# Kernel optimization log

Hardware: AMD Instinct MI355X
Metric: run time of the kernel (lower is better)

Reference implementation:

```python
import jax, jax.numpy as jnp
import numpy as np

N = 100000
E = 640000
D = 128


def _sage_conv(x, src, dst, Wp, bp, Wl, bl, Wr):
    # project=True: project + relu source features before aggregation
    h = jax.nn.relu(x @ Wp.T + bp)            # [N, D]
    msgs = h[src]                              # [E, D] gather
    summed = jax.ops.segment_sum(msgs, dst, num_segments=N)   # [N, D]
    cnt = jax.ops.segment_sum(jnp.ones((msgs.shape[0],), x.dtype), dst, num_segments=N)
    mean = summed / jnp.maximum(cnt, 1.0)[:, None]
    # lin_l on aggregated neighbors (with bias) + lin_r on root (no bias)
    return mean @ Wl.T + bl + x @ Wr.T


def setup_inputs() -> dict:
    key = jax.random.key(0)
    ks = jax.random.split(key, 16)
    s = 1.0 / np.sqrt(D)
    x = jax.random.normal(ks[0], (N, D), dtype=jnp.float32)
    edge_index = jax.random.randint(ks[1], (2, E), 0, N, dtype=jnp.int64)
    params = {}
    for i, base in enumerate(["conv0", "conv1"]):
        params[base + "_Wp"] = jax.random.uniform(ks[2 + 5 * i], (D, D), jnp.float32, -s, s)
        params[base + "_bp"] = jax.random.uniform(ks[3 + 5 * i], (D,), jnp.float32, -s, s)
        params[base + "_Wl"] = jax.random.uniform(ks[4 + 5 * i], (D, D), jnp.float32, -s, s)
        params[base + "_bl"] = jax.random.uniform(ks[5 + 5 * i], (D,), jnp.float32, -s, s)
        params[base + "_Wr"] = jax.random.uniform(ks[6 + 5 * i], (D, D), jnp.float32, -s, s)
    return {"x": x, "edge_index": edge_index, **params}


def reference(x, edge_index,
              conv0_Wp, conv0_bp, conv0_Wl, conv0_bl, conv0_Wr,
              conv1_Wp, conv1_bp, conv1_Wl, conv1_bl, conv1_Wr):
    src, dst = edge_index[0], edge_index[1]
    h = _sage_conv(x, src, dst, conv0_Wp, conv0_bp, conv0_Wl, conv0_bl, conv0_Wr)
    h = jax.nn.relu(h)
    return _sage_conv(h, src, dst, conv1_Wp, conv1_bp, conv1_Wl, conv1_bl, conv1_Wr)
```

## Files before the change

### kernel.cpp

```cpp
#include <hip/hip_runtime.h>

#define DD 128

typedef _Float16 f16;
typedef __attribute__((ext_vector_type(8))) _Float16 v8h;
typedef __attribute__((ext_vector_type(4))) _Float16 v4h;
typedef __attribute__((ext_vector_type(2))) _Float16 f16x2;
typedef __attribute__((ext_vector_type(4))) float f32x4;

static inline int cdiv(int a, int b) { return (a + b - 1) / b; }


__global__ __launch_bounds__(256) void zero_kernel(int* __restrict__ p, int n) {
    int i = blockIdx.x * 256 + threadIdx.x;
    if (i < n) p[i] = 0;
}


__global__ __launch_bounds__(256) void count_kernel(const int* __restrict__ dst, int E,
                                                    int* __restrict__ cnt) {
    int e = blockIdx.x * 256 + threadIdx.x;
    if (e < E) atomicAdd(&cnt[dst[e]], 1);
}

__global__ __launch_bounds__(256) void scan1(const int* __restrict__ cnt, int N,
                                             int* __restrict__ bsum) {
    __shared__ int s[256];
    int i = blockIdx.x * 256 + threadIdx.x;
    s[threadIdx.x] = (i < N) ? cnt[i] : 0;
    __syncthreads();
    for (int off = 128; off > 0; off >>= 1) {
        if (threadIdx.x < off) s[threadIdx.x] += s[threadIdx.x + off];
        __syncthreads();
    }
    if (threadIdx.x == 0) bsum[blockIdx.x] = s[0];
}

__global__ __launch_bounds__(512) void scan2(const int* __restrict__ bsum, int NB,
                                             int* __restrict__ boff) {
    __shared__ int s[512];
    int t = threadIdx.x;
    int v = (t < NB) ? bsum[t] : 0;
    s[t] = v;
    __syncthreads();
    for (int off = 1; off < 512; off <<= 1) {
        int x = (t >= off) ? s[t - off] : 0;
        __syncthreads();
        s[t] += x;
        __syncthreads();
    }
    if (t < NB) boff[t] = s[t] - v;
}

__global__ __launch_bounds__(256) void scan3(const int* __restrict__ cnt,
                                             const int* __restrict__ boff, int N,
                                             int* __restrict__ off) {
    __shared__ int s[256];
    int t = threadIdx.x;
    int i = blockIdx.x * 256 + t;
    int v = (i < N) ? cnt[i] : 0;
    s[t] = v;
    __syncthreads();
    for (int o = 1; o < 256; o <<= 1) {
        int x = (t >= o) ? s[t - o] : 0;
        __syncthreads();
        s[t] += x;
        __syncthreads();
    }
    int excl = s[t] - v + boff[blockIdx.x];
    if (i < N) off[i] = excl;
    if (i == N - 1) off[N] = excl + v;
}

__global__ __launch_bounds__(256) void fill_kernel(const int* __restrict__ src,
                                                   const int* __restrict__ dst, int E,
                                                   const int* __restrict__ off,
                                                   int* __restrict__ cnt,
                                                   int* __restrict__ csr) {
    int e = blockIdx.x * 256 + threadIdx.x;
    if (e < E) {
        int d = dst[e];
        int p = atomicSub(&cnt[d], 1) - 1;
        csr[off[d] + p] = src[e];
    }
}


__global__ __launch_bounds__(256) void cvt_w_kernel(const float* __restrict__ W0,
                                                    const float* __restrict__ W1,
                                                    const float* __restrict__ W2,
                                                    const float* __restrict__ W3,
                                                    const float* __restrict__ W4,
                                                    const float* __restrict__ W5,
                                                    f16* __restrict__ out) {
    int mat = blockIdx.x >> 4;
    const float* W = mat == 0 ? W0 : mat == 1 ? W1 : mat == 2 ? W2
                   : mat == 3 ? W3 : mat == 4 ? W4 : W5;
    int base = (blockIdx.x & 15) * 1024 + threadIdx.x * 4;
    float4 v = *(const float4*)(W + base);
    v4h o;
    o[0] = (f16)v.x; o[1] = (f16)v.y; o[2] = (f16)v.z; o[3] = (f16)v.w;
    *(v4h*)(out + mat * 16384 + base) = o;
}

__global__ __launch_bounds__(256) void cvt_x_kernel(const float* __restrict__ x,
                                                    f16* __restrict__ out, int n8) {
    int i = blockIdx.x * 256 + threadIdx.x;
    if (i >= n8) return;
    float4 a = *(const float4*)(x + (size_t)i * 8);
    float4 b = *(const float4*)(x + (size_t)i * 8 + 4);
    v8h r;
    r[0] = (f16)a.x; r[1] = (f16)a.y; r[2] = (f16)a.z; r[3] = (f16)a.w;
    r[4] = (f16)b.x; r[5] = (f16)b.y; r[6] = (f16)b.z; r[7] = (f16)b.w;
    *(v8h*)(out + (size_t)i * 8) = r;
}


__global__ __launch_bounds__(256) void aggregate_kernel(const f16* __restrict__ h,
                                                        const int* __restrict__ off,
                                                        const int* __restrict__ csr,
                                                        f16* __restrict__ mean, int N) {
    int n = blockIdx.x * 4 + (threadIdx.x >> 6);
    int l = threadIdx.x & 63;
    int g = l >> 4, c = l & 15;
    if (n >= N) return;
    int s = off[n], e = off[n + 1];
    float acc[8] = {0.f, 0.f, 0.f, 0.f, 0.f, 0.f, 0.f, 0.f};
    for (int i = s + g; i < e; i += 4) {
        int idx = csr[i];
        v8h v = *(const v8h*)(h + (size_t)idx * DD + c * 8);
#pragma unroll
        for (int j = 0; j < 8; ++j) acc[j] += (float)v[j];
    }
#pragma unroll
    for (int j = 0; j < 8; ++j) {
        acc[j] += __shfl_xor(acc[j], 16);
        acc[j] += __shfl_xor(acc[j], 32);
    }
    int deg = e - s;
    float inv = 1.0f / (float)(deg > 0 ? deg : 1);
    if (g == 0) {
        v8h o;
#pragma unroll
        for (int j = 0; j < 8; ++j) o[j] = (f16)(acc[j] * inv);
        *(v8h*)(mean + (size_t)n * DD + c * 8) = o;
    }
}


__device__ inline void stage_w(const f16* __restrict__ Wg, f16* __restrict__ smem, int t) {
#pragma unroll
    for (int i = 0; i < 8; ++i) {
        int idx16 = i * 256 + t;
        int col = idx16 >> 4, c16 = idx16 & 15;
        int sc = c16 ^ (col & 7);
        uint4 v = *(const uint4*)(Wg + idx16 * 8);
        *(uint4*)(smem + col * DD + sc * 8) = v;
    }
}

__device__ inline v8h read_b(const f16* __restrict__ smem, int ct, int ki, int l) {
    int col = ct * 16 + (l & 15);
    int c16 = ki * 4 + (l >> 4);
    int sc = c16 ^ (col & 7);
    return *(const v8h*)(smem + col * DD + sc * 8);
}

__device__ inline v8h load_frag16(const f16* __restrict__ A, int row, int kb, int M) {
    if (row >= M) {
        v8h z = {};
        return z;
    }
    return *(const v8h*)(A + (size_t)row * DD + kb);
}


__global__ __launch_bounds__(256) void proj_gemm(const f16* __restrict__ A,
                                                 const f16* __restrict__ W1,
                                                 const float* __restrict__ bias,
                                                 f16* __restrict__ OUT, int M) {
    __shared__ f16 WS[DD * DD];
    int t = threadIdx.x, l = t & 63, w = t >> 6;
    int row0 = blockIdx.x * 128 + w * 32;
    int r = l & 15, cg = l >> 4;

    stage_w(W1, WS, t);

    v8h af[2][4];
#pragma unroll
    for (int rt = 0; rt < 2; ++rt)
#pragma unroll
        for (int ki = 0; ki < 4; ++ki)
            af[rt][ki] = load_frag16(A, row0 + rt * 16 + r, ki * 32 + cg * 8, M);
    __syncthreads();

    f32x4 acc[2][8];
#pragma unroll
    for (int ct = 0; ct < 8; ++ct) {
        float bv = bias[ct * 16 + r];
        f32x4 b4 = {bv, bv, bv, bv};
        acc[0][ct] = b4;
        acc[1][ct] = b4;
    }

#pragma unroll
    for (int ct = 0; ct < 8; ++ct)
#pragma unroll
        for (int ki = 0; ki < 4; ++ki) {
            v8h b = read_b(WS, ct, ki, l);
            acc[0][ct] = __builtin_amdgcn_mfma_f32_16x16x32_f16(af[0][ki], b, acc[0][ct], 0, 0, 0);
            acc[1][ct] = __builtin_amdgcn_mfma_f32_16x16x32_f16(af[1][ki], b, acc[1][ct], 0, 0, 0);
        }

#pragma unroll
    for (int rt = 0; rt < 2; ++rt)
#pragma unroll
        for (int ct = 0; ct < 8; ++ct)
#pragma unroll
            for (int j = 0; j < 4; ++j) {
                int row = row0 + rt * 16 + cg * 4 + j;
                if (row < M)
                    OUT[(size_t)row * DD + ct * 16 + r] = (f16)fmaxf(acc[rt][ct][j], 0.f);
            }
}


template <typename TO, bool RELU>
__global__ __launch_bounds__(256) void dual_gemm(const f16* __restrict__ A,
                                                 const f16* __restrict__ Wl,
                                                 const float* __restrict__ bias,
                                                 const f16* __restrict__ B,
                                                 const f16* __restrict__ Wr,
                                                 TO* __restrict__ OUT, int M) {
    __shared__ f16 WS[DD * DD];
    int t = threadIdx.x, l = t & 63, w = t >> 6;
    int row0 = blockIdx.x * 128 + w * 32;
    int r = l & 15, cg = l >> 4;

    stage_w(Wl, WS, t);

    v8h afA[2][4], afB[2][4];
#pragma unroll
    for (int rt = 0; rt < 2; ++rt)
#pragma unroll
        for (int ki = 0; ki < 4; ++ki) {
            int row = row0 + rt * 16 + r, kb = ki * 32 + cg * 8;
            afA[rt][ki] = load_frag16(A, row, kb, M);
            afB[rt][ki] = load_frag16(B, row, kb, M);
        }
    __syncthreads();

    f32x4 acc[2][8];
#pragma unroll
    for (int ct = 0; ct < 8; ++ct) {
        float bv = bias[ct * 16 + r];
        f32x4 b4 = {bv, bv, bv, bv};
        acc[0][ct] = b4;
        acc[1][ct] = b4;
    }

#pragma unroll
    for (int ct = 0; ct < 8; ++ct)
#pragma unroll
        for (int ki = 0; ki < 4; ++ki) {
            v8h b = read_b(WS, ct, ki, l);
            acc[0][ct] = __builtin_amdgcn_mfma_f32_16x16x32_f16(afA[0][ki], b, acc[0][ct], 0, 0, 0);
            acc[1][ct] = __builtin_amdgcn_mfma_f32_16x16x32_f16(afA[1][ki], b, acc[1][ct], 0, 0, 0);
        }

    __syncthreads();
    stage_w(Wr, WS, t);
    __syncthreads();

#pragma unroll
    for (int ct = 0; ct < 8; ++ct)
#pragma unroll
        for (int ki = 0; ki < 4; ++ki) {
            v8h b = read_b(WS, ct, ki, l);
            acc[0][ct] = __builtin_amdgcn_mfma_f32_16x16x32_f16(afB[0][ki], b, acc[0][ct], 0, 0, 0);
            acc[1][ct] = __builtin_amdgcn_mfma_f32_16x16x32_f16(afB[1][ki], b, acc[1][ct], 0, 0, 0);
        }

#pragma unroll
    for (int rt = 0; rt < 2; ++rt)
#pragma unroll
        for (int ct = 0; ct < 8; ++ct)
#pragma unroll
            for (int j = 0; j < 4; ++j) {
                int row = row0 + rt * 16 + cg * 4 + j;
                if (row < M) {
                    float v = acc[rt][ct][j];
                    if (RELU) v = fmaxf(v, 0.f);
                    OUT[(size_t)row * DD + ct * 16 + r] = (TO)v;
                }
            }
}


__global__ __launch_bounds__(256) void dualproj_gemm(const f16* __restrict__ A,
                                                     const f16* __restrict__ Wl,
                                                     const float* __restrict__ bl,
                                                     const f16* __restrict__ B,
                                                     const f16* __restrict__ Wr,
                                                     f16* __restrict__ Y,
                                                     const f16* __restrict__ Wp,
                                                     const float* __restrict__ bp,
                                                     f16* __restrict__ H, int M) {
    __shared__ f16 WS[DD * DD];
    int t = threadIdx.x, l = t & 63, w = t >> 6;
    int row0 = blockIdx.x * 128 + w * 32;
    int r = l & 15, cg = l >> 4;

    stage_w(Wl, WS, t);

    v8h afA[2][4], afB[2][4];
#pragma unroll
    for (int rt = 0; rt < 2; ++rt)
#pragma unroll
        for (int ki = 0; ki < 4; ++ki) {
            int row = row0 + rt * 16 + r, kb = ki * 32 + cg * 8;
            afA[rt][ki] = load_frag16(A, row, kb, M);
            afB[rt][ki] = load_frag16(B, row, kb, M);
        }
    __syncthreads();

    f32x4 acc[2][8];
#pragma unroll
    for (int ct = 0; ct < 8; ++ct) {
        float bv = bl[ct * 16 + r];
        f32x4 b4 = {bv, bv, bv, bv};
        acc[0][ct] = b4;
        acc[1][ct] = b4;
    }

#pragma unroll
    for (int ct = 0; ct < 8; ++ct)
#pragma unroll
        for (int ki = 0; ki < 4; ++ki) {
            v8h b = read_b(WS, ct, ki, l);
            acc[0][ct] = __builtin_amdgcn_mfma_f32_16x16x32_f16(afA[0][ki], b, acc[0][ct], 0, 0, 0);
            acc[1][ct] = __builtin_amdgcn_mfma_f32_16x16x32_f16(afA[1][ki], b, acc[1][ct], 0, 0, 0);
        }

    __syncthreads();
    stage_w(Wr, WS, t);
    __syncthreads();

#pragma unroll
    for (int ct = 0; ct < 8; ++ct)
#pragma unroll
        for (int ki = 0; ki < 4; ++ki) {
            v8h b = read_b(WS, ct, ki, l);
            acc[0][ct] = __builtin_amdgcn_mfma_f32_16x16x32_f16(afB[0][ki], b, acc[0][ct], 0, 0, 0);
            acc[1][ct] = __builtin_amdgcn_mfma_f32_16x16x32_f16(afB[1][ki], b, acc[1][ct], 0, 0, 0);
        }

    __syncthreads();
#pragma unroll
    for (int rt = 0; rt < 2; ++rt)
#pragma unroll
        for (int ct = 0; ct < 8; ++ct)
#pragma unroll
            for (int j = 0; j < 4; ++j) {
                int brow = w * 32 + rt * 16 + cg * 4 + j;
                int col = ct * 16 + r;
                f16 hv = (f16)fmaxf(acc[rt][ct][j], 0.f);
                int c16 = col >> 3;
                WS[brow * DD + (((c16 ^ (brow & 7)) << 3) | (col & 7))] = hv;
                int grow = blockIdx.x * 128 + brow;
                if (grow < M) Y[(size_t)grow * DD + col] = hv;
            }
    __syncthreads();

    v8h af2[2][4];
#pragma unroll
    for (int rt = 0; rt < 2; ++rt)
#pragma unroll
        for (int ki = 0; ki < 4; ++ki) {
            int brow = w * 32 + rt * 16 + r;
            af2[rt][ki] = *(const v8h*)(WS + brow * DD + (((ki * 4 + cg) ^ (brow & 7)) << 3));
        }
    __syncthreads();

    stage_w(Wp, WS, t);

    f32x4 acc2[2][8];
#pragma unroll
    for (int ct = 0; ct < 8; ++ct) {
        float bv = bp[ct * 16 + r];
        f32x4 b4 = {bv, bv, bv, bv};
        acc2[0][ct] = b4;
        acc2[1][ct] = b4;
    }
    __syncthreads();

#pragma unroll
    for (int ct = 0; ct < 8; ++ct)
#pragma unroll
        for (int ki = 0; ki < 4; ++ki) {
            v8h b = read_b(WS, ct, ki, l);
            acc2[0][ct] = __builtin_amdgcn_mfma_f32_16x16x32_f16(af2[0][ki], b, acc2[0][ct], 0, 0, 0);
            acc2[1][ct] = __builtin_amdgcn_mfma_f32_16x16x32_f16(af2[1][ki], b, acc2[1][ct], 0, 0, 0);
        }

#pragma unroll
    for (int rt = 0; rt < 2; ++rt)
#pragma unroll
        for (int ct = 0; ct < 8; ++ct)
#pragma unroll
            for (int j = 0; j < 4; ++j) {
                int row = row0 + rt * 16 + cg * 4 + j;
                if (row < M)
                    H[(size_t)row * DD + ct * 16 + r] = (f16)fmaxf(acc2[rt][ct][j], 0.f);
            }
}


extern "C" void kernel_launch(void* const* d_in, const int* in_sizes, int n_in,
                              void* d_out, int out_size, void* d_ws, size_t ws_size,
                              hipStream_t stream) {
    const float* x = (const float*)d_in[0];
    const int* ei = (const int*)d_in[1];
    const float* Wp0 = (const float*)d_in[2];
    const float* bp0 = (const float*)d_in[3];
    const float* Wl0 = (const float*)d_in[4];
    const float* bl0 = (const float*)d_in[5];
    const float* Wr0 = (const float*)d_in[6];
    const float* Wp1 = (const float*)d_in[7];
    const float* bp1 = (const float*)d_in[8];
    const float* Wl1 = (const float*)d_in[9];
    const float* bl1 = (const float*)d_in[10];
    const float* Wr1 = (const float*)d_in[11];

    int N = in_sizes[0] / DD;
    int E = in_sizes[1] / 2;
    const int* src = ei;
    const int* dst = ei + E;

    char* ws = (char*)d_ws;
    size_t o = 0;
    auto alloc = [&](size_t bytes) {
        size_t r = o;
        o = (o + bytes + 255) & ~(size_t)255;
        return r;
    };
    f16* w16 = (f16*)(ws + alloc((size_t)6 * DD * DD * 2));
    int* cnt = (int*)(ws + alloc((size_t)N * 4));
    int* off = (int*)(ws + alloc((size_t)(N + 1) * 4));
    int NB = cdiv(N, 256);
    int* bsum = (int*)(ws + alloc((size_t)NB * 4));
    int* boff = (int*)(ws + alloc((size_t)NB * 4));
    int* csr = (int*)(ws + alloc((size_t)E * 4));
    f16* mean = (f16*)(ws + alloc((size_t)N * DD * 2));
    f16* y1 = (f16*)(ws + alloc((size_t)N * DD * 2));
    f16* h = (f16*)d_out;
    f16* x16 = (f16*)((char*)d_out + (size_t)N * DD * 2);
    (void)ws_size;

    zero_kernel<<<NB, 256, 0, stream>>>(cnt, N);
    count_kernel<<<cdiv(E, 256), 256, 0, stream>>>(dst, E, cnt);
    scan1<<<NB, 256, 0, stream>>>(cnt, N, bsum);
    scan2<<<1, 512, 0, stream>>>(bsum, NB, boff);
    scan3<<<NB, 256, 0, stream>>>(cnt, boff, N, off);
    fill_kernel<<<cdiv(E, 256), 256, 0, stream>>>(src, dst, E, off, cnt, csr);

    cvt_w_kernel<<<96, 256, 0, stream>>>(Wp0, Wl0, Wr0, Wp1, Wl1, Wr1, w16);
    const f16* wp0 = w16 + 0 * 16384;
    const f16* wl0 = w16 + 1 * 16384;
    const f16* wr0 = w16 + 2 * 16384;
    const f16* wp1 = w16 + 3 * 16384;
    const f16* wl1 = w16 + 4 * 16384;
    const f16* wr1 = w16 + 5 * 16384;

    cvt_x_kernel<<<cdiv(N * DD / 8, 256), 256, 0, stream>>>(x, x16, N * DD / 8);

    int GB = cdiv(N, 128);
    proj_gemm<<<GB, 256, 0, stream>>>(x16, wp0, bp0, h, N);
    aggregate_kernel<<<cdiv(N, 4), 256, 0, stream>>>(h, off, csr, mean, N);
    dualproj_gemm<<<GB, 256, 0, stream>>>(mean, wl0, bl0, x16, wr0, y1, wp1, bp1, h, N);
    aggregate_kernel<<<cdiv(N, 4), 256, 0, stream>>>(h, off, csr, mean, N);
    dual_gemm<float, false><<<GB, 256, 0, stream>>>(mean, wl1, bl1, y1, wr1, (float*)d_out, N);
}
```

Before: 243.0 us.

## Fuse CSR build and conversions into fewer launches with atomic-cursor offsets

After: 257.6 us. 6.0% more time.

```diff
diff --git a/kernel.cpp b/kernel.cpp
--- a/kernel.cpp
+++ b/kernel.cpp
@@ -5,7 +5,6 @@
 typedef _Float16 f16;
 typedef __attribute__((ext_vector_type(8))) _Float16 v8h;
 typedef __attribute__((ext_vector_type(4))) _Float16 v4h;
-typedef __attribute__((ext_vector_type(2))) _Float16 f16x2;
 typedef __attribute__((ext_vector_type(4))) float f32x4;
 
 static inline int cdiv(int a, int b) { return (a + b - 1) / b; }
@@ -17,45 +16,47 @@
 }
 
 
-__global__ __launch_bounds__(256) void count_kernel(const int* __restrict__ dst, int E,
-                                                    int* __restrict__ cnt) {
-    int e = blockIdx.x * 256 + threadIdx.x;
-    if (e < E) atomicAdd(&cnt[dst[e]], 1);
-}
-
-__global__ __launch_bounds__(256) void scan1(const int* __restrict__ cnt, int N,
-                                             int* __restrict__ bsum) {
+__global__ __launch_bounds__(256) void bigprep_kernel(
+    const float* __restrict__ x, f16* __restrict__ x16, int n8,
+    const float* __restrict__ W0, const float* __restrict__ W1,
+    const float* __restrict__ W2, const float* __restrict__ W3,
+    const float* __restrict__ W4, const float* __restrict__ W5,
+    f16* __restrict__ w16,
+    const int* __restrict__ dst, int E, int* __restrict__ cnt,
+    int nbx) {
+    int b = blockIdx.x;
+    if (b < nbx) {
+        int i = b * 256 + threadIdx.x;
+        if (i >= n8) return;
+        float4 a = *(const float4*)(x + (size_t)i * 8);
+        float4 c = *(const float4*)(x + (size_t)i * 8 + 4);
+        v8h r;
+        r[0] = (f16)a.x; r[1] = (f16)a.y; r[2] = (f16)a.z; r[3] = (f16)a.w;
+        r[4] = (f16)c.x; r[5] = (f16)c.y; r[6] = (f16)c.z; r[7] = (f16)c.w;
+        *(v8h*)(x16 + (size_t)i * 8) = r;
+    } else if (b < nbx + 96) {
+        int bb = b - nbx;
+        int mat = bb >> 4;
+        const float* W = mat == 0 ? W0 : mat == 1 ? W1 : mat == 2 ? W2
+                       : mat == 3 ? W3 : mat == 4 ? W4 : W5;
+        int base = (bb & 15) * 1024 + threadIdx.x * 4;
+        float4 v = *(const float4*)(W + base);
+        v4h o;
+        o[0] = (f16)v.x; o[1] = (f16)v.y; o[2] = (f16)v.z; o[3] = (f16)v.w;
+        *(v4h*)(w16 + mat * 16384 + base) = o;
+    } else {
+        int e = (b - nbx - 96) * 256 + threadIdx.x;
+        if (e < E) atomicAdd(&cnt[dst[e]], 1);
+    }
+}
+
+
+__global__ __launch_bounds__(256) void offs_kernel(const int* __restrict__ cnt, int N,
+                                                   int* __restrict__ off,
+                                                   int* __restrict__ deg,
+                                                   int* __restrict__ cursor) {
     __shared__ int s[256];
-    int i = blockIdx.x * 256 + threadIdx.x;
-    s[threadIdx.x] = (i < N) ? cnt[i] : 0;
-    __syncthreads();
-    for (int off = 128; off > 0; off >>= 1) {
-        if (threadIdx.x < off) s[threadIdx.x] += s[threadIdx.x + off];
-        __syncthreads();
-    }
-    if (threadIdx.x == 0) bsum[blockIdx.x] = s[0];
-}
-
-__global__ __launch_bounds__(512) void scan2(const int* __restrict__ bsum, int NB,
-                                             int* __restrict__ boff) {
-    __shared__ int s[512];
-    int t = threadIdx.x;
-    int v = (t < NB) ? bsum[t] : 0;
-    s[t] = v;
-    __syncthreads();
-    for (int off = 1; off < 512; off <<= 1) {
-        int x = (t >= off) ? s[t - off] : 0;
-        __syncthreads();
-        s[t] += x;
-        __syncthreads();
-    }
-    if (t < NB) boff[t] = s[t] - v;
-}
-
-__global__ __launch_bounds__(256) void scan3(const int* __restrict__ cnt,
-                                             const int* __restrict__ boff, int N,
-                                             int* __restrict__ off) {
-    __shared__ int s[256];
+    __shared__ int base;
     int t = threadIdx.x;
     int i = blockIdx.x * 256 + t;
     int v = (i < N) ? cnt[i] : 0;
@@ -67,64 +68,112 @@
         s[t] += x;
         __syncthreads();
     }
-    int excl = s[t] - v + boff[blockIdx.x];
-    if (i < N) off[i] = excl;
-    if (i == N - 1) off[N] = excl + v;
-}
-
-__global__ __launch_bounds__(256) void fill_kernel(const int* __restrict__ src,
-                                                   const int* __restrict__ dst, int E,
-                                                   const int* __restrict__ off,
-                                                   int* __restrict__ cnt,
-                                                   int* __restrict__ csr) {
-    int e = blockIdx.x * 256 + threadIdx.x;
-    if (e < E) {
-        int d = dst[e];
-        int p = atomicSub(&cnt[d], 1) - 1;
-        csr[off[d] + p] = src[e];
-    }
-}
-
-
-__global__ __launch_bounds__(256) void cvt_w_kernel(const float* __restrict__ W0,
-                                                    const float* __restrict__ W1,
-                                                    const float* __restrict__ W2,
-                                                    const float* __restrict__ W3,
-                                                    const float* __restrict__ W4,
-                                                    const float* __restrict__ W5,
-                                                    f16* __restrict__ out) {
-    int mat = blockIdx.x >> 4;
-    const float* W = mat == 0 ? W0 : mat == 1 ? W1 : mat == 2 ? W2
-                   : mat == 3 ? W3 : mat == 4 ? W4 : W5;
-    int base = (blockIdx.x & 15) * 1024 + threadIdx.x * 4;
-    float4 v = *(const float4*)(W + base);
-    v4h o;
-    o[0] = (f16)v.x; o[1] = (f16)v.y; o[2] = (f16)v.z; o[3] = (f16)v.w;
-    *(v4h*)(out + mat * 16384 + base) = o;
-}
-
-__global__ __launch_bounds__(256) void cvt_x_kernel(const float* __restrict__ x,
-                                                    f16* __restrict__ out, int n8) {
-    int i = blockIdx.x * 256 + threadIdx.x;
-    if (i >= n8) return;
-    float4 a = *(const float4*)(x + (size_t)i * 8);
-    float4 b = *(const float4*)(x + (size_t)i * 8 + 4);
-    v8h r;
-    r[0] = (f16)a.x; r[1] = (f16)a.y; r[2] = (f16)a.z; r[3] = (f16)a.w;
-    r[4] = (f16)b.x; r[5] = (f16)b.y; r[6] = (f16)b.z; r[7] = (f16)b.w;
-    *(v8h*)(out + (size_t)i * 8) = r;
+    if (t == 255) base = atomicAdd(cursor, s[255]);
+    __syncthreads();
+    if (i < N) {
+        off[i] = base + s[t] - v;
+        deg[i] = v;
+    }
+}
+
+
+__device__ inline void stage_w(const f16* __restrict__ Wg, f16* __restrict__ smem, int t) {
+#pragma unroll
+    for (int i = 0; i < 8; ++i) {
+        int idx16 = i * 256 + t;
+        int col = idx16 >> 4, c16 = idx16 & 15;
+        int sc = c16 ^ (col & 7);
+        uint4 v = *(const uint4*)(Wg + idx16 * 8);
+        *(uint4*)(smem + col * DD + sc * 8) = v;
+    }
+}
+
+__device__ inline v8h read_b(const f16* __restrict__ smem, int ct, int ki, int l) {
+    int col = ct * 16 + (l & 15);
+    int c16 = ki * 4 + (l >> 4);
+    int sc = c16 ^ (col & 7);
+    return *(const v8h*)(smem + col * DD + sc * 8);
+}
+
+__device__ inline v8h load_frag16(const f16* __restrict__ A, int row, int kb, int M) {
+    if (row >= M) {
+        v8h z = {};
+        return z;
+    }
+    return *(const v8h*)(A + (size_t)row * DD + kb);
+}
+
+
+__global__ __launch_bounds__(256) void fuse1_kernel(
+    const f16* __restrict__ A, const f16* __restrict__ W1,
+    const float* __restrict__ bias, f16* __restrict__ OUT, int M, int GB,
+    const int* __restrict__ src, const int* __restrict__ dst, int E,
+    const int* __restrict__ off, int* __restrict__ cnt, int* __restrict__ csr) {
+    __shared__ f16 WS[DD * DD];
+    if (blockIdx.x >= (unsigned)GB) {
+        int e = (blockIdx.x - GB) * 256 + threadIdx.x;
+        if (e < E) {
+            int d = dst[e];
+            int p = atomicSub(&cnt[d], 1) - 1;
+            csr[off[d] + p] = src[e];
+        }
+        return;
+    }
+    int t = threadIdx.x, l = t & 63, w = t >> 6;
+    int row0 = blockIdx.x * 128 + w * 32;
+    int r = l & 15, cg = l >> 4;
+
+    stage_w(W1, WS, t);
+
+    v8h af[2][4];
+#pragma unroll
+    for (int rt = 0; rt < 2; ++rt)
+#pragma unroll
+        for (int ki = 0; ki < 4; ++ki)
+            af[rt][ki] = load_frag16(A, row0 + rt * 16 + r, ki * 32 + cg * 8, M);
+    __syncthreads();
+
+    f32x4 acc[2][8];
+#pragma unroll
+    for (int ct = 0; ct < 8; ++ct) {
+        float bv = bias[ct * 16 + r];
+        f32x4 b4 = {bv, bv, bv, bv};
+        acc[0][ct] = b4;
+        acc[1][ct] = b4;
+    }
+
+#pragma unroll
+    for (int ct = 0; ct < 8; ++ct)
+#pragma unroll
+        for (int ki = 0; ki < 4; ++ki) {
+            v8h b = read_b(WS, ct, ki, l);
+            acc[0][ct] = __builtin_amdgcn_mfma_f32_16x16x32_f16(af[0][ki], b, acc[0][ct], 0, 0, 0);
+            acc[1][ct] = __builtin_amdgcn_mfma_f32_16x16x32_f16(af[1][ki], b, acc[1][ct], 0, 0, 0);
+        }
+
+#pragma unroll
+    for (int rt = 0; rt < 2; ++rt)
+#pragma unroll
+        for (int ct = 0; ct < 8; ++ct)
+#pragma unroll
+            for (int j = 0; j < 4; ++j) {
+                int row = row0 + rt * 16 + cg * 4 + j;
+                if (row < M)
+                    OUT[(size_t)row * DD + ct * 16 + r] = (f16)fmaxf(acc[rt][ct][j], 0.f);
+            }
 }
 
 
 __global__ __launch_bounds__(256) void aggregate_kernel(const f16* __restrict__ h,
                                                         const int* __restrict__ off,
+                                                        const int* __restrict__ deg,
                                                         const int* __restrict__ csr,
                                                         f16* __restrict__ mean, int N) {
     int n = blockIdx.x * 4 + (threadIdx.x >> 6);
     int l = threadIdx.x & 63;
     int g = l >> 4, c = l & 15;
     if (n >= N) return;
-    int s = off[n], e = off[n + 1];
+    int s = off[n], d = deg[n], e = s + d;
     float acc[8] = {0.f, 0.f, 0.f, 0.f, 0.f, 0.f, 0.f, 0.f};
     for (int i = s + g; i < e; i += 4) {
         int idx = csr[i];
@@ -137,91 +186,13 @@
         acc[j] += __shfl_xor(acc[j], 16);
         acc[j] += __shfl_xor(acc[j], 32);
     }
-    int deg = e - s;
-    float inv = 1.0f / (float)(deg > 0 ? deg : 1);
+    float inv = 1.0f / (float)(d > 0 ? d : 1);
     if (g == 0) {
         v8h o;
 #pragma unroll
         for (int j = 0; j < 8; ++j) o[j] = (f16)(acc[j] * inv);
         *(v8h*)(mean + (size_t)n * DD + c * 8) = o;
     }
-}
-
-
-__device__ inline void stage_w(const f16* __restrict__ Wg, f16* __restrict__ smem, int t) {
-#pragma unroll
-    for (int i = 0; i < 8; ++i) {
-        int idx16 = i * 256 + t;
-        int col = idx16 >> 4, c16 = idx16 & 15;
-        int sc = c16 ^ (col & 7);
-        uint4 v = *(const uint4*)(Wg + idx16 * 8);
-        *(uint4*)(smem + col * DD + sc * 8) = v;
-    }
-}
-
-__device__ inline v8h read_b(const f16* __restrict__ smem, int ct, int ki, int l) {
-    int col = ct * 16 + (l & 15);
-    int c16 = ki * 4 + (l >> 4);
-    int sc = c16 ^ (col & 7);
-    return *(const v8h*)(smem + col * DD + sc * 8);
-}
-
-__device__ inline v8h load_frag16(const f16* __restrict__ A, int row, int kb, int M) {
-    if (row >= M) {
-        v8h z = {};
-        return z;
-    }
-    return *(const v8h*)(A + (size_t)row * DD + kb);
-}
-
-
-__global__ __launch_bounds__(256) void proj_gemm(const f16* __restrict__ A,
-                                                 const f16* __restrict__ W1,
-                                                 const float* __restrict__ bias,
-                                                 f16* __restrict__ OUT, int M) {
-    __shared__ f16 WS[DD * DD];
-    int t = threadIdx.x, l = t & 63, w = t >> 6;
-    int row0 = blockIdx.x * 128 + w * 32;
-    int r = l & 15, cg = l >> 4;
-
-    stage_w(W1, WS, t);
-
-    v8h af[2][4];
-#pragma unroll
-    for (int rt = 0; rt < 2; ++rt)
-#pragma unroll
-        for (int ki = 0; ki < 4; ++ki)
-            af[rt][ki] = load_frag16(A, row0 + rt * 16 + r, ki * 32 + cg * 8, M);
-    __syncthreads();
-
-    f32x4 acc[2][8];
-#pragma unroll
-    for (int ct = 0; ct < 8; ++ct) {
-        float bv = bias[ct * 16 + r];
-        f32x4 b4 = {bv, bv, bv, bv};
-        acc[0][ct] = b4;
-        acc[1][ct] = b4;
-    }
-
-#pragma unroll
-    for (int ct = 0; ct < 8; ++ct)
-#pragma unroll
-        for (int ki = 0; ki < 4; ++ki) {
-            v8h b = read_b(WS, ct, ki, l);
-            acc[0][ct] = __builtin_amdgcn_mfma_f32_16x16x32_f16(af[0][ki], b, acc[0][ct], 0, 0, 0);
-            acc[1][ct] = __builtin_amdgcn_mfma_f32_16x16x32_f16(af[1][ki], b, acc[1][ct], 0, 0, 0);
-        }
-
-#pragma unroll
-    for (int rt = 0; rt < 2; ++rt)
-#pragma unroll
-        for (int ct = 0; ct < 8; ++ct)
-#pragma unroll
-            for (int j = 0; j < 4; ++j) {
-                int row = row0 + rt * 16 + cg * 4 + j;
-                if (row < M)
-                    OUT[(size_t)row * DD + ct * 16 + r] = (f16)fmaxf(acc[rt][ct][j], 0.f);
-            }
 }
 
 
@@ -445,11 +416,9 @@
         return r;
     };
     f16* w16 = (f16*)(ws + alloc((size_t)6 * DD * DD * 2));
-    int* cnt = (int*)(ws + alloc((size_t)N * 4));
-    int* off = (int*)(ws + alloc((size_t)(N + 1) * 4));
-    int NB = cdiv(N, 256);
-    int* bsum = (int*)(ws + alloc((size_t)NB * 4));
-    int* boff = (int*)(ws + alloc((size_t)NB * 4));
+    int* cnt = (int*)(ws + alloc((size_t)(N + 1) * 4));
+    int* off = (int*)(ws + alloc((size_t)N * 4));
+    int* deg = (int*)(ws + alloc((size_t)N * 4));
     int* csr = (int*)(ws + alloc((size_t)E * 4));
     f16* mean = (f16*)(ws + alloc((size_t)N * DD * 2));
     f16* y1 = (f16*)(ws + alloc((size_t)N * DD * 2));
@@ -457,14 +426,12 @@
     f16* x16 = (f16*)((char*)d_out + (size_t)N * DD * 2);
     (void)ws_size;
 
-    zero_kernel<<<NB, 256, 0, stream>>>(cnt, N);
-    count_kernel<<<cdiv(E, 256), 256, 0, stream>>>(dst, E, cnt);
-    scan1<<<NB, 256, 0, stream>>>(cnt, N, bsum);
-    scan2<<<1, 512, 0, stream>>>(bsum, NB, boff);
-    scan3<<<NB, 256, 0, stream>>>(cnt, boff, N, off);
-    fill_kernel<<<cdiv(E, 256), 256, 0, stream>>>(src, dst, E, off, cnt, csr);
-
-    cvt_w_kernel<<<96, 256, 0, stream>>>(Wp0, Wl0, Wr0, Wp1, Wl1, Wr1, w16);
+    int NB = cdiv(N, 256);
+    int EB = cdiv(E, 256);
+    int n8 = N * DD / 8;
+    int nbx = cdiv(n8, 256);
+    int GB = cdiv(N, 128);
+
     const f16* wp0 = w16 + 0 * 16384;
     const f16* wl0 = w16 + 1 * 16384;
     const f16* wr0 = w16 + 2 * 16384;
@@ -472,12 +439,14 @@
     const f16* wl1 = w16 + 4 * 16384;
     const f16* wr1 = w16 + 5 * 16384;
 
-    cvt_x_kernel<<<cdiv(N * DD / 8, 256), 256, 0, stream>>>(x, x16, N * DD / 8);
-
-    int GB = cdiv(N, 128);
-    proj_gemm<<<GB, 256, 0, stream>>>(x16, wp0, bp0, h, N);
-    aggregate_kernel<<<cdiv(N, 4), 256, 0, stream>>>(h, off, csr, mean, N);
+    zero_kernel<<<cdiv(N + 1, 256), 256, 0, stream>>>(cnt, N + 1);
+    bigprep_kernel<<<nbx + 96 + EB, 256, 0, stream>>>(
+        x, x16, n8, Wp0, Wl0, Wr0, Wp1, Wl1, Wr1, w16, dst, E, cnt, nbx);
+    offs_kernel<<<NB, 256, 0, stream>>>(cnt, N, off, deg, &cnt[N]);
+    fuse1_kernel<<<GB + EB, 256, 0, stream>>>(x16, wp0, bp0, h, N, GB,
+                                              src, dst, E, off, cnt, csr);
+    aggregate_kernel<<<cdiv(N, 4), 256, 0, stream>>>(h, off, deg, csr, mean, N);
     dualproj_gemm<<<GB, 256, 0, stream>>>(mean, wl0, bl0, x16, wr0, y1, wp1, bp1, h, N);
-    aggregate_kernel<<<cdiv(N, 4), 256, 0, stream>>>(h, off, csr, mean, N);
+    aggregate_kernel<<<cdiv(N, 4), 256, 0, stream>>>(h, off, deg, csr, mean, N);
     dual_gemm<float, false><<<GB, 256, 0, stream>>>(mean, wl1, bl1, y1, wr1, (float*)d_out, N);
 }
```
